# Kernel optimization log

Measured on AMD Instinct MI355X. Metric: run time of the kernel, lower is better.

## Reference

```python
import jax, jax.numpy as jnp
import numpy as np
from jax import lax

T = 2048          # tokens (batch*seq, module flattens to [-1, hidden])
H = 2048          # hidden_size
E = 32            # n_routed_experts
DF = 1024         # moe_intermediate_size
DS = 4096         # moe_shared_expert_intermediate_size
TOP_K = 6         # num_experts_per_tok
N_GROUP = 8
TOPK_GROUP = 4
SCALE = 2.5       # routed_scaling_factor
NORM_TOPK = True


def relu2(x):
    r = jax.nn.relu(x)
    return r * r


def setup_inputs() -> dict:
    key = jax.random.key(0)
    ks = jax.random.split(key, 7)
    s = 0.02
    return {
        "x": jax.random.normal(ks[0], (T, H), dtype=jnp.float32),
        "router_w": jax.random.normal(ks[1], (E, H), dtype=jnp.float32) * s,
        "router_b": jax.random.normal(ks[2], (E,), dtype=jnp.float32) * s,
        "w_up": jax.random.normal(ks[3], (E, H, DF), dtype=jnp.float32) * s,
        "w_down": jax.random.normal(ks[4], (E, DF, H), dtype=jnp.float32) * s,
        "shared_up": jax.random.normal(ks[5], (H, DS), dtype=jnp.float32) * s,
        "shared_down": jax.random.normal(ks[6], (DS, H), dtype=jnp.float32) * s,
    }


def _route(x, router_w, router_b):
    # router in fp32: logits -> sigmoid scores -> group-restricted top-k
    logits = x @ router_w.T                                  # [T, E]
    scores = jax.nn.sigmoid(logits)
    sfc = scores + router_b[None, :]                         # scores_for_choice
    gsize = E // N_GROUP
    grp = sfc.reshape(T, N_GROUP, gsize)
    group_scores = lax.top_k(grp, 2)[0].sum(-1)              # [T, n_group] sum of top-2
    _, gidx = lax.top_k(group_scores, TOPK_GROUP)            # [T, topk_group]
    group_mask = jax.nn.one_hot(gidx, N_GROUP, dtype=sfc.dtype).sum(1)  # [T, n_group]
    score_mask = jnp.repeat(group_mask, gsize, axis=1)       # [T, E]
    masked = jnp.where(score_mask > 0, sfc, 0.0)
    _, tidx = lax.top_k(masked, TOP_K)                       # [T, top_k]
    tw = jnp.take_along_axis(scores, tidx, axis=1)           # gather raw scores
    if NORM_TOPK:
        tw = tw / (tw.sum(-1, keepdims=True) + 1e-20)
    tw = tw * SCALE
    return tidx, tw


def reference(x, router_w, router_b, w_up, w_down, shared_up, shared_down):
    tidx, tw = _route(x, router_w, router_b)
    # dense combine weights [T, E]; equals sum of routed weights per expert
    combine = (jax.nn.one_hot(tidx, E, dtype=tw.dtype) * tw[..., None]).sum(1)
    # routed experts (no bias, so scaling before down_proj == scaling the output)
    h = jnp.einsum('td,edf->tef', x, w_up)                   # [T, E, DF]
    a = relu2(h) * combine[:, :, None]
    moe_out = jnp.einsum('tef,efd->td', a, w_down)           # [T, H]
    shared_out = relu2(x @ shared_up) @ shared_down
    return moe_out + shared_out
```

## Files before the change

kernel.cpp:

```cpp
#include <hip/hip_runtime.h>
#include <hip/hip_bf16.h>
#include <math.h>

#define T_TOK 2048
#define HID   2048
#define NE    32
#define DF    1024
#define DSZ   4096
#define TOPK  6
#define NGRP  8
#define TOPKG 4
#define RSCALE 2.5f
#define EXT_E 36
#define NSLOT 20480

typedef __attribute__((ext_vector_type(8))) short short8;
typedef __attribute__((ext_vector_type(4))) float f32x4;

typedef __attribute__((address_space(1))) const void gv1;
typedef __attribute__((address_space(3))) void lv3;

static __device__ __forceinline__ void gload16(const void* g, void* l) {
    __builtin_amdgcn_global_load_lds((gv1*)g, (lv3*)l, 16, 0, 0);
}

static __device__ __forceinline__ unsigned short f2b(float f) {
    union { float f; unsigned u; } v; v.f = f;
    unsigned r = v.u + 0x7fffu + ((v.u >> 16) & 1u);
    return (unsigned short)(r >> 16);
}

static __device__ __forceinline__ float b2f(unsigned short b) {
    union { float f; unsigned u; } v; v.u = ((unsigned)b) << 16;
    return v.f;
}

__global__ __launch_bounds__(256)
void router_kernel(const float* __restrict__ x, const float* __restrict__ rw,
                   const float* __restrict__ rb,
                   int* __restrict__ tidx, float* __restrict__ tw,
                   int* __restrict__ counts, unsigned short* __restrict__ xb) {
    __shared__ float xs[HID];
    __shared__ float part[256];
    __shared__ float scores[NE];
    __shared__ float sfc[NE];
    int t = blockIdx.x;
    int tid = threadIdx.x;
    for (int i = tid; i < HID / 4; i += 256) {
        ((float4*)xs)[i] = ((const float4*)(x + (size_t)t * HID))[i];
    }
    __syncthreads();
    {
        float4 a = ((const float4*)xs)[tid * 2];
        float4 b = ((const float4*)xs)[tid * 2 + 1];
        short8 o;
        o[0] = (short)f2b(a.x); o[1] = (short)f2b(a.y); o[2] = (short)f2b(a.z); o[3] = (short)f2b(a.w);
        o[4] = (short)f2b(b.x); o[5] = (short)f2b(b.y); o[6] = (short)f2b(b.z); o[7] = (short)f2b(b.w);
        *(short8*)(xb + (size_t)t * HID + tid * 8) = o;
    }
    int e = tid & 31, ch = tid >> 5;
    const float* w = rw + (size_t)e * HID + ch * 256;
    const float* xv = xs + ch * 256;
    float p = 0.f;
    #pragma unroll 8
    for (int k = 0; k < 256; ++k) p += xv[k] * w[k];
    part[tid] = p;
    __syncthreads();
    if (tid < 32) {
        float l = 0.f;
        #pragma unroll
        for (int c = 0; c < 8; ++c) l += part[c * 32 + tid];
        float s = 1.f / (1.f + expf(-l));
        scores[tid] = s;
        sfc[tid] = s + rb[tid];
    }
    __syncthreads();
    if (tid == 0) {
        float gs[NGRP];
        for (int g = 0; g < NGRP; ++g) {
            float v[4];
            for (int i = 0; i < 4; ++i) v[i] = sfc[g * 4 + i];
            int bi = 0;
            for (int i = 1; i < 4; ++i) if (v[i] > v[bi]) bi = i;
            float m1 = v[bi]; v[bi] = -INFINITY;
            int bj = 0;
            for (int i = 1; i < 4; ++i) if (v[i] > v[bj]) bj = i;
            gs[g] = m1 + v[bj];
        }
        bool gsel[NGRP];
        for (int g = 0; g < NGRP; ++g) gsel[g] = false;
        for (int k = 0; k < TOPKG; ++k) {
            int bi = -1; float b = -INFINITY;
            for (int g = 0; g < NGRP; ++g)
                if (!gsel[g] && gs[g] > b) { b = gs[g]; bi = g; }
            gsel[bi] = true;
        }
        float masked[NE];
        for (int i = 0; i < NE; ++i) masked[i] = gsel[i >> 2] ? sfc[i] : 0.0f;
        int sel[TOPK]; float wv[TOPK]; float wsum = 0.f;
        for (int k = 0; k < TOPK; ++k) {
            int bi = -1; float b = -INFINITY;
            for (int i = 0; i < NE; ++i)
                if (masked[i] > b) { b = masked[i]; bi = i; }
            masked[bi] = -INFINITY;
            sel[k] = bi; wv[k] = scores[bi]; wsum += wv[k];
        }
        float inv = RSCALE / (wsum + 1e-20f);
        for (int k = 0; k < TOPK; ++k) {
            tidx[t * TOPK + k] = sel[k];
            tw[t * TOPK + k] = wv[k] * inv;
            atomicAdd(&counts[sel[k]], 1);
        }
    }
}

__global__ void scan_kernel(const int* __restrict__ counts, int* __restrict__ offsets) {
    if (threadIdx.x == 0) {
        int a = 0;
        for (int e2 = 0; e2 < NE; ++e2) { offsets[e2] = a; a += counts[e2]; }
        offsets[NE] = a;
        for (int j = 1; j <= 4; ++j) offsets[NE + j] = 12288 + j * T_TOK;
    }
}

__global__ void scatter_kernel(const int* __restrict__ tidx, const float* __restrict__ tw,
                               const int* __restrict__ offsets, int* __restrict__ cursors,
                               int* __restrict__ perm, float* __restrict__ pw,
                               int* __restrict__ slot_of) {
    int t = blockIdx.x * blockDim.x + threadIdx.x;
    if (t >= T_TOK) return;
    for (int k = 0; k < TOPK; ++k) {
        int e = tidx[t * TOPK + k];
        int pos = atomicAdd(&cursors[e], 1);
        int slot = offsets[e] + pos;
        perm[slot] = t;
        pw[slot] = tw[t * TOPK + k];
        slot_of[t * TOPK + k] = slot;
    }
    #pragma unroll
    for (int j = 0; j < 4; ++j) {
        int slot = 12288 + j * T_TOK + t;
        perm[slot] = t;
        pw[slot] = 1.0f;
    }
}

static __device__ __forceinline__ void transpose_tile64(
        const float* __restrict__ src, unsigned short* __restrict__ dst,
        int rs, int Kd, int k0, int n0) {
    __shared__ float tl[64][65];
    int t = threadIdx.x;
    int r0 = t >> 4;
    int c4 = (t & 15) * 4;
    #pragma unroll
    for (int p = 0; p < 4; ++p) {
        int r = r0 + p * 16;
        float4 v = *(const float4*)(src + (size_t)(k0 + r) * rs + n0 + c4);
        tl[c4 + 0][r] = v.x;
        tl[c4 + 1][r] = v.y;
        tl[c4 + 2][r] = v.z;
        tl[c4 + 3][r] = v.w;
    }
    __syncthreads();
    int n = t >> 2;
    int kq = (t & 3) * 16;
    unsigned short o[16];
    #pragma unroll
    for (int i = 0; i < 16; ++i) o[i] = f2b(tl[n][kq + i]);
    unsigned short* d = dst + (size_t)(n0 + n) * Kd + k0 + kq;
    *(short8*)(d) = *(short8*)&o[0];
    *(short8*)(d + 8) = *(short8*)&o[8];
}

__global__ __launch_bounds__(256)
void transpose_all_kernel(const float* __restrict__ w_up, const float* __restrict__ sh_up,
                          const float* __restrict__ w_dn, const float* __restrict__ sh_dn,
                          unsigned short* __restrict__ bufU, unsigned short* __restrict__ bufD) {
    int z = blockIdx.y;
    int tile = blockIdx.x;
    if (z < EXT_E) {
        const float* src; int rs;
        if (z < NE) { src = w_up + (size_t)z * HID * DF; rs = DF; }
        else        { src = sh_up + (size_t)(z - NE) * DF; rs = DSZ; }
        int tn = tile & 15, tk = tile >> 4;
        transpose_tile64(src, bufU + (size_t)z * DF * HID, rs, HID, tk * 64, tn * 64);
    } else {
        int zz = z - EXT_E;
        const float* src = (zz < NE) ? (w_dn + (size_t)zz * DF * HID)
                                     : (sh_dn + (size_t)(zz - NE) * DF * HID);
        int tn = tile & 31, tk = tile >> 5;
        transpose_tile64(src, bufD + (size_t)zz * HID * DF, HID, DF, tk * 64, tn * 64);
    }
}

__global__ __launch_bounds__(256, 2)
void gemm_up_kernel(const unsigned short* __restrict__ xb, const unsigned short* __restrict__ bufU,
                    unsigned short* __restrict__ act, const int* __restrict__ offsets,
                    const int* __restrict__ perm, const float* __restrict__ pw) {
    constexpr int K = HID, N = DF;
    __shared__ __align__(16) char lds[32768];
    char* As = lds;
    char* Bs = lds + 16384;

    int tid = threadIdx.x;
    int lane = tid & 63, wvid = tid >> 6, wr = wvid >> 1, wc = wvid & 1;

    int bz = blockIdx.z;
    int off = offsets[bz], end = offsets[bz + 1];
    int row0 = off + blockIdx.y * 128;
    if (row0 >= end) return;
    int n0 = blockIdx.x * 128;

    int lr = lane >> 3;
    int csrc = (((lane & 7) ^ lr) << 4);
    size_t abyte[4], bbyte[4];
    int ldsoff[4];
    const char* Bb = (const char*)bufU + (size_t)bz * ((size_t)N * K * 2);
    #pragma unroll
    for (int p = 0; p < 4; ++p) {
        int r = p * 32 + wvid * 8 + lr;
        int gr = row0 + r;
        if (gr > end - 1) gr = end - 1;
        abyte[p] = (size_t)perm[gr] * (K * 2);
        bbyte[p] = (size_t)(n0 + r) * (K * 2);
        ldsoff[p] = (p * 32 + wvid * 8) * 128;
    }

    f32x4 acc[4][4] = {};
    for (int k0 = 0; k0 < K; k0 += 64) {
        __syncthreads();
        #pragma unroll
        for (int p = 0; p < 4; ++p) {
            gload16((const char*)xb + abyte[p] + k0 * 2 + csrc, As + ldsoff[p]);
            gload16(Bb + bbyte[p] + k0 * 2 + csrc, Bs + ldsoff[p]);
        }
        __syncthreads();
        #pragma unroll
        for (int ks = 0; ks < 2; ++ks) {
            int kg = lane >> 4, r16 = lane & 15;
            short8 af[4], bfr[4];
            #pragma unroll
            for (int m = 0; m < 4; ++m) {
                int r = wr * 64 + m * 16 + r16;
                af[m] = *(const short8*)(As + r * 128 + ((ks * 64 + kg * 16) ^ ((r & 7) << 4)));
            }
            #pragma unroll
            for (int n = 0; n < 4; ++n) {
                int c = wc * 64 + n * 16 + r16;
                bfr[n] = *(const short8*)(Bs + c * 128 + ((ks * 64 + kg * 16) ^ ((c & 7) << 4)));
            }
            #pragma unroll
            for (int m = 0; m < 4; ++m)
                #pragma unroll
                for (int n = 0; n < 4; ++n)
                    acc[m][n] = __builtin_amdgcn_mfma_f32_16x16x32_bf16(af[m], bfr[n], acc[m][n], 0, 0, 0);
        }
    }

    int r16 = lane & 15, rg = lane >> 4;
    #pragma unroll
    for (int m = 0; m < 4; ++m) {
        #pragma unroll
        for (int j = 0; j < 4; ++j) {
            int rr = row0 + wr * 64 + m * 16 + rg * 4 + j;
            if (rr < end) {
                float scale = pw[rr];
                #pragma unroll
                for (int n = 0; n < 4; ++n) {
                    int cc = n0 + wc * 64 + n * 16 + r16;
                    float v = acc[m][n][j];
                    v = v > 0.f ? v * v : 0.f;
                    act[(size_t)rr * N + cc] = f2b(v * scale);
                }
            }
        }
    }
}

__global__ __launch_bounds__(256, 2)
void gemm_down_kernel(const unsigned short* __restrict__ act, const unsigned short* __restrict__ bufD,
                      unsigned short* __restrict__ slotout, const int* __restrict__ offsets) {
    constexpr int K = DF, N = HID;
    __shared__ __align__(16) char lds[32768];
    char* As = lds;
    char* Bs = lds + 16384;

    int tid = threadIdx.x;
    int lane = tid & 63, wvid = tid >> 6, wr = wvid >> 1, wc = wvid & 1;

    int bz = blockIdx.z;
    int off = offsets[bz], end = offsets[bz + 1];
    int row0 = off + blockIdx.y * 128;
    if (row0 >= end) return;
    int n0 = blockIdx.x * 128;

    int lr = lane >> 3;
    int csrc = (((lane & 7) ^ lr) << 4);
    size_t abyte[4], bbyte[4];
    int ldsoff[4];
    const char* Bb = (const char*)bufD + (size_t)bz * ((size_t)N * K * 2);
    #pragma unroll
    for (int p = 0; p < 4; ++p) {
        int r = p * 32 + wvid * 8 + lr;
        int gr = row0 + r;
        if (gr > end - 1) gr = end - 1;
        abyte[p] = (size_t)gr * (K * 2);
        bbyte[p] = (size_t)(n0 + r) * (K * 2);
        ldsoff[p] = (p * 32 + wvid * 8) * 128;
    }

    f32x4 acc[4][4] = {};
    for (int k0 = 0; k0 < K; k0 += 64) {
        __syncthreads();
        #pragma unroll
        for (int p = 0; p < 4; ++p) {
            gload16((const char*)act + abyte[p] + k0 * 2 + csrc, As + ldsoff[p]);
            gload16(Bb + bbyte[p] + k0 * 2 + csrc, Bs + ldsoff[p]);
        }
        __syncthreads();
        #pragma unroll
        for (int ks = 0; ks < 2; ++ks) {
            int kg = lane >> 4, r16 = lane & 15;
            short8 af[4], bfr[4];
            #pragma unroll
            for (int m = 0; m < 4; ++m) {
                int r = wr * 64 + m * 16 + r16;
                af[m] = *(const short8*)(As + r * 128 + ((ks * 64 + kg * 16) ^ ((r & 7) << 4)));
            }
            #pragma unroll
            for (int n = 0; n < 4; ++n) {
                int c = wc * 64 + n * 16 + r16;
                bfr[n] = *(const short8*)(Bs + c * 128 + ((ks * 64 + kg * 16) ^ ((c & 7) << 4)));
            }
            #pragma unroll
            for (int m = 0; m < 4; ++m)
                #pragma unroll
                for (int n = 0; n < 4; ++n)
                    acc[m][n] = __builtin_amdgcn_mfma_f32_16x16x32_bf16(af[m], bfr[n], acc[m][n], 0, 0, 0);
        }
    }

    int r16 = lane & 15, rg = lane >> 4;
    #pragma unroll
    for (int m = 0; m < 4; ++m) {
        #pragma unroll
        for (int j = 0; j < 4; ++j) {
            int rr = row0 + wr * 64 + m * 16 + rg * 4 + j;
            if (rr < end) {
                #pragma unroll
                for (int n = 0; n < 4; ++n) {
                    int cc = n0 + wc * 64 + n * 16 + r16;
                    slotout[(size_t)rr * N + cc] = f2b(acc[m][n][j]);
                }
            }
        }
    }
}

__global__ void combine_kernel(const unsigned short* __restrict__ slotout,
                               const int* __restrict__ slot_of,
                               float* __restrict__ out) {
    int t = blockIdx.x, tid = threadIdx.x;
    int s[10];
    #pragma unroll
    for (int k = 0; k < TOPK; ++k) s[k] = slot_of[t * TOPK + k];
    #pragma unroll
    for (int j = 0; j < 4; ++j) s[TOPK + j] = 12288 + j * T_TOK + t;
    int c = tid * 8;
    float a[8] = {0.f, 0.f, 0.f, 0.f, 0.f, 0.f, 0.f, 0.f};
    #pragma unroll
    for (int k = 0; k < 10; ++k) {
        short8 v = *(const short8*)(slotout + (size_t)s[k] * HID + c);
        #pragma unroll
        for (int i = 0; i < 8; ++i) a[i] += b2f((unsigned short)v[i]);
    }
    *(float4*)(out + (size_t)t * HID + c) = make_float4(a[0], a[1], a[2], a[3]);
    *(float4*)(out + (size_t)t * HID + c + 4) = make_float4(a[4], a[5], a[6], a[7]);
}

extern "C" void kernel_launch(void* const* d_in, const int* in_sizes, int n_in,
                              void* d_out, int out_size, void* d_ws, size_t ws_size,
                              hipStream_t stream) {
    const float* x     = (const float*)d_in[0];
    const float* rw    = (const float*)d_in[1];
    const float* rb    = (const float*)d_in[2];
    const float* w_up  = (const float*)d_in[3];
    const float* w_dn  = (const float*)d_in[4];
    const float* sh_up = (const float*)d_in[5];
    const float* sh_dn = (const float*)d_in[6];
    float* out = (float*)d_out;
    char* ws = (char*)d_ws;

    int*   counts  = (int*)(ws);
    int*   cursors = (int*)(ws + 128);
    int*   offsets = (int*)(ws + 256);
    int*   tidx    = (int*)(ws + 1024);
    float* tw      = (float*)(ws + 50176);
    int*   slot_of = (int*)(ws + 99328);
    int*   perm    = (int*)(ws + 148480);
    float* pw      = (float*)(ws + 230400);
    unsigned short* xb   = (unsigned short*)(ws + 312320);
    unsigned short* act  = (unsigned short*)(ws + 8700928);
    unsigned short* bufU = (unsigned short*)(ws + 50643968);
    unsigned short* bufD = (unsigned short*)(ws + 201638912);
    unsigned short* slotout = (unsigned short*)(ws + 352633856);

    hipMemsetAsync(ws, 0, 256, stream);

    router_kernel<<<T_TOK, 256, 0, stream>>>(x, rw, rb, tidx, tw, counts, xb);
    scan_kernel<<<1, 64, 0, stream>>>(counts, offsets);
    scatter_kernel<<<(T_TOK + 255) / 256, 256, 0, stream>>>(tidx, tw, offsets, cursors,
                                                            perm, pw, slot_of);

    transpose_all_kernel<<<dim3(512, 2 * EXT_E), 256, 0, stream>>>(
        w_up, sh_up, w_dn, sh_dn, bufU, bufD);

    gemm_up_kernel<<<dim3(DF / 128, T_TOK / 128, EXT_E), 256, 0, stream>>>(
        xb, bufU, act, offsets, perm, pw);

    gemm_down_kernel<<<dim3(HID / 128, T_TOK / 128, EXT_E), 256, 0, stream>>>(
        act, bufD, slotout, offsets);

    combine_kernel<<<T_TOK, 256, 0, stream>>>(slotout, slot_of, out);
}
```

Before: 572.8 us.

## Fuse weight fp32-to-bf16 conversion into GEMMs using transposed LDS reads

Removes the separate transpose/convert pass over all expert and shared weights. Each GEMM now loads fp32 weight tiles directly, converts them to bf16 in registers, stores them row-major in LDS, and uses ds_read_b64_tr_b16 to produce the transposed MFMA B fragments. This avoids writing and rereading about 300MB of bf16 weight copies. In exchange, each GEMM block rereads fp32 weights, which doubles B-operand load bytes per tile and repeats the conversion across row tiles. B loads also become synchronous register loads instead of direct global-to-LDS loads.

Result: slower. 680.6 us (+18.8%).

```diff
diff --git a/kernel.cpp b/kernel.cpp
--- a/kernel.cpp
+++ b/kernel.cpp
@@ -15,6 +15,7 @@
 #define NSLOT 20480
 
 typedef __attribute__((ext_vector_type(8))) short short8;
+typedef __attribute__((ext_vector_type(4))) short short4v;
 typedef __attribute__((ext_vector_type(4))) float f32x4;
 
 typedef __attribute__((address_space(1))) const void gv1;
@@ -28,6 +29,12 @@
     union { float f; unsigned u; } v; v.f = f;
     unsigned r = v.u + 0x7fffu + ((v.u >> 16) & 1u);
     return (unsigned short)(r >> 16);
+}
+
+static __device__ __forceinline__ unsigned short b16(float f) {
+    union { __hip_bfloat16 h; unsigned short u; } c;
+    c.h = __float2bfloat16(f);
+    return c.u;
 }
 
 static __device__ __forceinline__ float b2f(unsigned short b) {
@@ -145,59 +152,14 @@
     }
 }
 
-static __device__ __forceinline__ void transpose_tile64(
-        const float* __restrict__ src, unsigned short* __restrict__ dst,
-        int rs, int Kd, int k0, int n0) {
-    __shared__ float tl[64][65];
-    int t = threadIdx.x;
-    int r0 = t >> 4;
-    int c4 = (t & 15) * 4;
-    #pragma unroll
-    for (int p = 0; p < 4; ++p) {
-        int r = r0 + p * 16;
-        float4 v = *(const float4*)(src + (size_t)(k0 + r) * rs + n0 + c4);
-        tl[c4 + 0][r] = v.x;
-        tl[c4 + 1][r] = v.y;
-        tl[c4 + 2][r] = v.z;
-        tl[c4 + 3][r] = v.w;
-    }
-    __syncthreads();
-    int n = t >> 2;
-    int kq = (t & 3) * 16;
-    unsigned short o[16];
-    #pragma unroll
-    for (int i = 0; i < 16; ++i) o[i] = f2b(tl[n][kq + i]);
-    unsigned short* d = dst + (size_t)(n0 + n) * Kd + k0 + kq;
-    *(short8*)(d) = *(short8*)&o[0];
-    *(short8*)(d + 8) = *(short8*)&o[8];
-}
-
-__global__ __launch_bounds__(256)
-void transpose_all_kernel(const float* __restrict__ w_up, const float* __restrict__ sh_up,
-                          const float* __restrict__ w_dn, const float* __restrict__ sh_dn,
-                          unsigned short* __restrict__ bufU, unsigned short* __restrict__ bufD) {
-    int z = blockIdx.y;
-    int tile = blockIdx.x;
-    if (z < EXT_E) {
-        const float* src; int rs;
-        if (z < NE) { src = w_up + (size_t)z * HID * DF; rs = DF; }
-        else        { src = sh_up + (size_t)(z - NE) * DF; rs = DSZ; }
-        int tn = tile & 15, tk = tile >> 4;
-        transpose_tile64(src, bufU + (size_t)z * DF * HID, rs, HID, tk * 64, tn * 64);
-    } else {
-        int zz = z - EXT_E;
-        const float* src = (zz < NE) ? (w_dn + (size_t)zz * DF * HID)
-                                     : (sh_dn + (size_t)(zz - NE) * DF * HID);
-        int tn = tile & 31, tk = tile >> 5;
-        transpose_tile64(src, bufD + (size_t)zz * HID * DF, HID, DF, tk * 64, tn * 64);
-    }
-}
-
+template<int MODE>
 __global__ __launch_bounds__(256, 2)
-void gemm_up_kernel(const unsigned short* __restrict__ xb, const unsigned short* __restrict__ bufU,
-                    unsigned short* __restrict__ act, const int* __restrict__ offsets,
+void gemm_tr_kernel(const unsigned short* __restrict__ Abuf,
+                    const float* __restrict__ Wmain, const float* __restrict__ Wsh,
+                    unsigned short* __restrict__ Cbuf, const int* __restrict__ offsets,
                     const int* __restrict__ perm, const float* __restrict__ pw) {
-    constexpr int K = HID, N = DF;
+    constexpr int K = (MODE == 0) ? HID : DF;
+    constexpr int N = (MODE == 0) ? DF : HID;
     __shared__ __align__(16) char lds[32768];
     char* As = lds;
     char* Bs = lds + 16384;
@@ -211,49 +173,80 @@
     if (row0 >= end) return;
     int n0 = blockIdx.x * 128;
 
+    const float* Bsrc; long ldb;
+    if (MODE == 0) {
+        if (bz < NE) { Bsrc = Wmain + (size_t)bz * HID * DF; ldb = DF; }
+        else         { Bsrc = Wsh + (size_t)(bz - NE) * DF;  ldb = DSZ; }
+    } else {
+        Bsrc = (bz < NE) ? (Wmain + (size_t)bz * DF * HID)
+                         : (Wsh + (size_t)(bz - NE) * DF * HID);
+        ldb = HID;
+    }
+
     int lr = lane >> 3;
     int csrc = (((lane & 7) ^ lr) << 4);
-    size_t abyte[4], bbyte[4];
+    size_t abyte[4];
     int ldsoff[4];
-    const char* Bb = (const char*)bufU + (size_t)bz * ((size_t)N * K * 2);
     #pragma unroll
     for (int p = 0; p < 4; ++p) {
         int r = p * 32 + wvid * 8 + lr;
         int gr = row0 + r;
         if (gr > end - 1) gr = end - 1;
-        abyte[p] = (size_t)perm[gr] * (K * 2);
-        bbyte[p] = (size_t)(n0 + r) * (K * 2);
+        int s = (MODE == 0) ? perm[gr] : gr;
+        abyte[p] = (size_t)s * (K * 2);
         ldsoff[p] = (p * 32 + wvid * 8) * 128;
     }
+
+    int kr0 = (tid & 3) + ((tid >> 6) & 1) * 4;
+    int nc  = ((tid >> 2) & 15) * 4 + (tid >> 7) * 64;
+    int bwbase = (kr0 >> 2) * 1024 + (nc >> 4) * 128 + (kr0 & 3) * 32 + (nc & 15) * 2;
+
+    unsigned bsb = (unsigned)(uintptr_t)(lv3*)Bs + (unsigned)((lane >> 4) * 2048 + (lane & 15) * 8);
 
     f32x4 acc[4][4] = {};
     for (int k0 = 0; k0 < K; k0 += 64) {
         __syncthreads();
         #pragma unroll
-        for (int p = 0; p < 4; ++p) {
-            gload16((const char*)xb + abyte[p] + k0 * 2 + csrc, As + ldsoff[p]);
-            gload16(Bb + bbyte[p] + k0 * 2 + csrc, Bs + ldsoff[p]);
+        for (int p = 0; p < 4; ++p)
+            gload16((const char*)Abuf + abyte[p] + k0 * 2 + csrc, As + ldsoff[p]);
+        {
+            const float* bp = Bsrc + (size_t)(k0 + kr0) * ldb + n0 + nc;
+            #pragma unroll
+            for (int p = 0; p < 8; ++p) {
+                float4 v = *(const float4*)(bp + (size_t)p * 8 * ldb);
+                unsigned short h[4] = { b16(v.x), b16(v.y), b16(v.z), b16(v.w) };
+                *(short4v*)(Bs + bwbase + p * 2048) = *(short4v*)h;
+            }
         }
         __syncthreads();
         #pragma unroll
         for (int ks = 0; ks < 2; ++ks) {
-            int kg = lane >> 4, r16 = lane & 15;
-            short8 af[4], bfr[4];
+            int r16 = lane & 15, kg = lane >> 4;
+            short8 af[4];
             #pragma unroll
             for (int m = 0; m < 4; ++m) {
                 int r = wr * 64 + m * 16 + r16;
                 af[m] = *(const short8*)(As + r * 128 + ((ks * 64 + kg * 16) ^ ((r & 7) << 4)));
             }
+            short4v t0[4], t1[4];
             #pragma unroll
             for (int n = 0; n < 4; ++n) {
-                int c = wc * 64 + n * 16 + r16;
-                bfr[n] = *(const short8*)(Bs + c * 128 + ((ks * 64 + kg * 16) ^ ((c & 7) << 4)));
-            }
+                unsigned a = bsb + ks * 8192 + (wc * 4 + n) * 128;
+                asm volatile("ds_read_b64_tr_b16 %0, %2\n\t"
+                             "ds_read_b64_tr_b16 %1, %2 offset:1024"
+                             : "=v"(t0[n]), "=v"(t1[n]) : "v"(a));
+            }
+            asm volatile("s_waitcnt lgkmcnt(0)" ::: "memory");
+            __builtin_amdgcn_sched_barrier(0);
             #pragma unroll
-            for (int m = 0; m < 4; ++m)
+            for (int n = 0; n < 4; ++n) {
+                short8 bfr;
+                bfr[0] = t0[n][0]; bfr[1] = t0[n][1]; bfr[2] = t0[n][2]; bfr[3] = t0[n][3];
+                bfr[4] = t1[n][0]; bfr[5] = t1[n][1]; bfr[6] = t1[n][2]; bfr[7] = t1[n][3];
                 #pragma unroll
-                for (int n = 0; n < 4; ++n)
-                    acc[m][n] = __builtin_amdgcn_mfma_f32_16x16x32_bf16(af[m], bfr[n], acc[m][n], 0, 0, 0);
+                for (int m = 0; m < 4; ++m)
+                    acc[m][n] = __builtin_amdgcn_mfma_f32_16x16x32_bf16(af[m], bfr, acc[m][n], 0, 0, 0);
+            }
         }
     }
 
@@ -264,93 +257,21 @@
         for (int j = 0; j < 4; ++j) {
             int rr = row0 + wr * 64 + m * 16 + rg * 4 + j;
             if (rr < end) {
-                float scale = pw[rr];
-                #pragma unroll
-                for (int n = 0; n < 4; ++n) {
-                    int cc = n0 + wc * 64 + n * 16 + r16;
-                    float v = acc[m][n][j];
-                    v = v > 0.f ? v * v : 0.f;
-                    act[(size_t)rr * N + cc] = f2b(v * scale);
-                }
-            }
-        }
-    }
-}
-
-__global__ __launch_bounds__(256, 2)
-void gemm_down_kernel(const unsigned short* __restrict__ act, const unsigned short* __restrict__ bufD,
-                      unsigned short* __restrict__ slotout, const int* __restrict__ offsets) {
-    constexpr int K = DF, N = HID;
-    __shared__ __align__(16) char lds[32768];
-    char* As = lds;
-    char* Bs = lds + 16384;
-
-    int tid = threadIdx.x;
-    int lane = tid & 63, wvid = tid >> 6, wr = wvid >> 1, wc = wvid & 1;
-
-    int bz = blockIdx.z;
-    int off = offsets[bz], end = offsets[bz + 1];
-    int row0 = off + blockIdx.y * 128;
-    if (row0 >= end) return;
-    int n0 = blockIdx.x * 128;
-
-    int lr = lane >> 3;
-    int csrc = (((lane & 7) ^ lr) << 4);
-    size_t abyte[4], bbyte[4];
-    int ldsoff[4];
-    const char* Bb = (const char*)bufD + (size_t)bz * ((size_t)N * K * 2);
-    #pragma unroll
-    for (int p = 0; p < 4; ++p) {
-        int r = p * 32 + wvid * 8 + lr;
-        int gr = row0 + r;
-        if (gr > end - 1) gr = end - 1;
-        abyte[p] = (size_t)gr * (K * 2);
-        bbyte[p] = (size_t)(n0 + r) * (K * 2);
-        ldsoff[p] = (p * 32 + wvid * 8) * 128;
-    }
-
-    f32x4 acc[4][4] = {};
-    for (int k0 = 0; k0 < K; k0 += 64) {
-        __syncthreads();
-        #pragma unroll
-        for (int p = 0; p < 4; ++p) {
-            gload16((const char*)act + abyte[p] + k0 * 2 + csrc, As + ldsoff[p]);
-            gload16(Bb + bbyte[p] + k0 * 2 + csrc, Bs + ldsoff[p]);
-        }
-        __syncthreads();
-        #pragma unroll
-        for (int ks = 0; ks < 2; ++ks) {
-            int kg = lane >> 4, r16 = lane & 15;
-            short8 af[4], bfr[4];
-            #pragma unroll
-            for (int m = 0; m < 4; ++m) {
-                int r = wr * 64 + m * 16 + r16;
-                af[m] = *(const short8*)(As + r * 128 + ((ks * 64 + kg * 16) ^ ((r & 7) << 4)));
-            }
-            #pragma unroll
-            for (int n = 0; n < 4; ++n) {
-                int c = wc * 64 + n * 16 + r16;
-                bfr[n] = *(const short8*)(Bs + c * 128 + ((ks * 64 + kg * 16) ^ ((c & 7) << 4)));
-            }
-            #pragma unroll
-            for (int m = 0; m < 4; ++m)
-                #pragma unroll
-                for (int n = 0; n < 4; ++n)
-                    acc[m][n] = __builtin_amdgcn_mfma_f32_16x16x32_bf16(af[m], bfr[n], acc[m][n], 0, 0, 0);
-        }
-    }
-
-    int r16 = lane & 15, rg = lane >> 4;
-    #pragma unroll
-    for (int m = 0; m < 4; ++m) {
-        #pragma unroll
-        for (int j = 0; j < 4; ++j) {
-            int rr = row0 + wr * 64 + m * 16 + rg * 4 + j;
-            if (rr < end) {
-                #pragma unroll
-                for (int n = 0; n < 4; ++n) {
-                    int cc = n0 + wc * 64 + n * 16 + r16;
-                    slotout[(size_t)rr * N + cc] = f2b(acc[m][n][j]);
+                if (MODE == 0) {
+                    float scale = pw[rr];
+                    #pragma unroll
+                    for (int n = 0; n < 4; ++n) {
+                        int cc = n0 + wc * 64 + n * 16 + r16;
+                        float v = acc[m][n][j];
+                        v = v > 0.f ? v * v : 0.f;
+                        Cbuf[(size_t)rr * N + cc] = f2b(v * scale);
+                    }
+                } else {
+                    #pragma unroll
+                    for (int n = 0; n < 4; ++n) {
+                        int cc = n0 + wc * 64 + n * 16 + r16;
+                        Cbuf[(size_t)rr * N + cc] = f2b(acc[m][n][j]);
+                    }
                 }
             }
         }
@@ -401,9 +322,7 @@
     float* pw      = (float*)(ws + 230400);
     unsigned short* xb   = (unsigned short*)(ws + 312320);
     unsigned short* act  = (unsigned short*)(ws + 8700928);
-    unsigned short* bufU = (unsigned short*)(ws + 50643968);
-    unsigned short* bufD = (unsigned short*)(ws + 201638912);
-    unsigned short* slotout = (unsigned short*)(ws + 352633856);
+    unsigned short* slotout = (unsigned short*)(ws + 50643968);
 
     hipMemsetAsync(ws, 0, 256, stream);
 
@@ -412,14 +331,11 @@
     scatter_kernel<<<(T_TOK + 255) / 256, 256, 0, stream>>>(tidx, tw, offsets, cursors,
                                                             perm, pw, slot_of);
 
-    transpose_all_kernel<<<dim3(512, 2 * EXT_E), 256, 0, stream>>>(
-        w_up, sh_up, w_dn, sh_dn, bufU, bufD);
-
-    gemm_up_kernel<<<dim3(DF / 128, T_TOK / 128, EXT_E), 256, 0, stream>>>(
-        xb, bufU, act, offsets, perm, pw);
-
-    gemm_down_kernel<<<dim3(HID / 128, T_TOK / 128, EXT_E), 256, 0, stream>>>(
-        act, bufD, slotout, offsets);
+    gemm_tr_kernel<0><<<dim3(DF / 128, T_TOK / 128, EXT_E), 256, 0, stream>>>(
+        xb, w_up, sh_up, act, offsets, perm, pw);
+
+    gemm_tr_kernel<1><<<dim3(HID / 128, T_TOK / 128, EXT_E), 256, 0, stream>>>(
+        act, w_dn, sh_dn, slotout, offsets, perm, pw);
 
     combine_kernel<<<T_TOK, 256, 0, stream>>>(slotout, slot_of, out);
 }
```

## Double-buffer LDS tiles in up and down expert GEMMs to overlap loads

Applied to the files above, without the earlier changes.

Both grouped GEMM kernels now use two 32KB LDS buffers. The next K-tile is prefetched with global_load_lds while MFMAs run on the current tile, which hides global memory latency and leaves one barrier per iteration instead of two. The cost is twice the LDS per block (64KB), which may limit occupancy below the two blocks requested in launch bounds. Correctness relies on the trailing barrier waiting for the async LDS loads to finish.

New measurement: 614.7 us. 7.3% more time.

```diff
diff --git a/kernel.cpp b/kernel.cpp
--- a/kernel.cpp
+++ b/kernel.cpp
@@ -198,9 +198,7 @@
                     unsigned short* __restrict__ act, const int* __restrict__ offsets,
                     const int* __restrict__ perm, const float* __restrict__ pw) {
     constexpr int K = HID, N = DF;
-    __shared__ __align__(16) char lds[32768];
-    char* As = lds;
-    char* Bs = lds + 16384;
+    __shared__ __align__(16) char lds[65536];
 
     int tid = threadIdx.x;
     int lane = tid & 63, wvid = tid >> 6, wr = wvid >> 1, wc = wvid & 1;
@@ -227,14 +225,27 @@
     }
 
     f32x4 acc[4][4] = {};
-    for (int k0 = 0; k0 < K; k0 += 64) {
-        __syncthreads();
-        #pragma unroll
-        for (int p = 0; p < 4; ++p) {
-            gload16((const char*)xb + abyte[p] + k0 * 2 + csrc, As + ldsoff[p]);
-            gload16(Bb + bbyte[p] + k0 * 2 + csrc, Bs + ldsoff[p]);
-        }
-        __syncthreads();
+    constexpr int NT = K / 64;
+    int cur = 0;
+    #pragma unroll
+    for (int p = 0; p < 4; ++p) {
+        gload16((const char*)xb + abyte[p] + csrc, lds + ldsoff[p]);
+        gload16(Bb + bbyte[p] + csrc, lds + 16384 + ldsoff[p]);
+    }
+    __syncthreads();
+
+    for (int t = 0; t < NT; ++t) {
+        char* As = lds + cur * 32768;
+        char* Bs = As + 16384;
+        if (t + 1 < NT) {
+            int k2 = (t + 1) * 128;
+            char* Ad = lds + (cur ^ 1) * 32768;
+            #pragma unroll
+            for (int p = 0; p < 4; ++p) {
+                gload16((const char*)xb + abyte[p] + k2 + csrc, Ad + ldsoff[p]);
+                gload16(Bb + bbyte[p] + k2 + csrc, Ad + 16384 + ldsoff[p]);
+            }
+        }
         #pragma unroll
         for (int ks = 0; ks < 2; ++ks) {
             int kg = lane >> 4, r16 = lane & 15;
@@ -255,6 +266,8 @@
                 for (int n = 0; n < 4; ++n)
                     acc[m][n] = __builtin_amdgcn_mfma_f32_16x16x32_bf16(af[m], bfr[n], acc[m][n], 0, 0, 0);
         }
+        __syncthreads();
+        cur ^= 1;
     }
 
     int r16 = lane & 15, rg = lane >> 4;
@@ -281,9 +294,7 @@
 void gemm_down_kernel(const unsigned short* __restrict__ act, const unsigned short* __restrict__ bufD,
                       unsigned short* __restrict__ slotout, const int* __restrict__ offsets) {
     constexpr int K = DF, N = HID;
-    __shared__ __align__(16) char lds[32768];
-    char* As = lds;
-    char* Bs = lds + 16384;
+    __shared__ __align__(16) char lds[65536];
 
     int tid = threadIdx.x;
     int lane = tid & 63, wvid = tid >> 6, wr = wvid >> 1, wc = wvid & 1;
@@ -310,14 +321,27 @@
     }
 
     f32x4 acc[4][4] = {};
-    for (int k0 = 0; k0 < K; k0 += 64) {
-        __syncthreads();
-        #pragma unroll
-        for (int p = 0; p < 4; ++p) {
-            gload16((const char*)act + abyte[p] + k0 * 2 + csrc, As + ldsoff[p]);
-            gload16(Bb + bbyte[p] + k0 * 2 + csrc, Bs + ldsoff[p]);
-        }
-        __syncthreads();
+    constexpr int NT = K / 64;
+    int cur = 0;
+    #pragma unroll
+    for (int p = 0; p < 4; ++p) {
+        gload16((const char*)act + abyte[p] + csrc, lds + ldsoff[p]);
+        gload16(Bb + bbyte[p] + csrc, lds + 16384 + ldsoff[p]);
+    }
+    __syncthreads();
+
+    for (int t = 0; t < NT; ++t) {
+        char* As = lds + cur * 32768;
+        char* Bs = As + 16384;
+        if (t + 1 < NT) {
+            int k2 = (t + 1) * 128;
+            char* Ad = lds + (cur ^ 1) * 32768;
+            #pragma unroll
+            for (int p = 0; p < 4; ++p) {
+                gload16((const char*)act + abyte[p] + k2 + csrc, Ad + ldsoff[p]);
+                gload16(Bb + bbyte[p] + k2 + csrc, Ad + 16384 + ldsoff[p]);
+            }
+        }
         #pragma unroll
         for (int ks = 0; ks < 2; ++ks) {
             int kg = lane >> 4, r16 = lane & 15;
@@ -338,6 +362,8 @@
                 for (int n = 0; n < 4; ++n)
                     acc[m][n] = __builtin_amdgcn_mfma_f32_16x16x32_bf16(af[m], bfr[n], acc[m][n], 0, 0, 0);
         }
+        __syncthreads();
+        cur ^= 1;
     }
 
     int r16 = lane & 15, rg = lane >> 4;
```

## Overlap down-weight transpose with up-projection GEMM in one interleaved launch

Applied to the files above, without the earlier changes.

Splits the weight transpose so that only the up-projection weights are transposed before the up GEMM. The down-projection transpose tiles are interleaved with up-GEMM tiles in a single fused launch, four transpose blocks per GEMM block. The goal is to overlap the memory-bound fp32-to-bf16 transpose with the compute-bound GEMM and remove one launch plus its serialization. The cost is a shared LDS allocation sized for the GEMM, which may lower transpose occupancy, and mixed block types that could unbalance scheduling.

Measured after the change: 564.3 us, median of 2. About the same (-1.5%).

```diff
diff --git a/kernel.cpp b/kernel.cpp
--- a/kernel.cpp
+++ b/kernel.cpp
@@ -147,8 +147,8 @@
 
 static __device__ __forceinline__ void transpose_tile64(
         const float* __restrict__ src, unsigned short* __restrict__ dst,
-        int rs, int Kd, int k0, int n0) {
-    __shared__ float tl[64][65];
+        int rs, int Kd, int k0, int n0, char* smem) {
+    float (*tl)[65] = (float(*)[65])smem;
     int t = threadIdx.x;
     int r0 = t >> 4;
     int c4 = (t & 15) * 4;
@@ -173,43 +173,36 @@
 }
 
 __global__ __launch_bounds__(256)
-void transpose_all_kernel(const float* __restrict__ w_up, const float* __restrict__ sh_up,
-                          const float* __restrict__ w_dn, const float* __restrict__ sh_dn,
-                          unsigned short* __restrict__ bufU, unsigned short* __restrict__ bufD) {
+void transpose_up_kernel(const float* __restrict__ w_up, const float* __restrict__ sh_up,
+                         unsigned short* __restrict__ bufU) {
+    __shared__ __align__(16) char smem[16640];
     int z = blockIdx.y;
+    const float* src; int rs;
+    if (z < NE) { src = w_up + (size_t)z * HID * DF; rs = DF; }
+    else        { src = sh_up + (size_t)(z - NE) * DF; rs = DSZ; }
     int tile = blockIdx.x;
-    if (z < EXT_E) {
-        const float* src; int rs;
-        if (z < NE) { src = w_up + (size_t)z * HID * DF; rs = DF; }
-        else        { src = sh_up + (size_t)(z - NE) * DF; rs = DSZ; }
-        int tn = tile & 15, tk = tile >> 4;
-        transpose_tile64(src, bufU + (size_t)z * DF * HID, rs, HID, tk * 64, tn * 64);
-    } else {
-        int zz = z - EXT_E;
-        const float* src = (zz < NE) ? (w_dn + (size_t)zz * DF * HID)
-                                     : (sh_dn + (size_t)(zz - NE) * DF * HID);
-        int tn = tile & 31, tk = tile >> 5;
-        transpose_tile64(src, bufD + (size_t)zz * HID * DF, HID, DF, tk * 64, tn * 64);
-    }
-}
-
-__global__ __launch_bounds__(256, 2)
-void gemm_up_kernel(const unsigned short* __restrict__ xb, const unsigned short* __restrict__ bufU,
-                    unsigned short* __restrict__ act, const int* __restrict__ offsets,
-                    const int* __restrict__ perm, const float* __restrict__ pw) {
+    int tn = tile & 15, tk = tile >> 4;
+    transpose_tile64(src, bufU + (size_t)z * DF * HID, rs, HID, tk * 64, tn * 64, smem);
+}
+
+static __device__ void gemm_up_body(int bx, int by, int bz,
+                                    const unsigned short* __restrict__ xb,
+                                    const unsigned short* __restrict__ bufU,
+                                    unsigned short* __restrict__ act,
+                                    const int* __restrict__ offsets,
+                                    const int* __restrict__ perm,
+                                    const float* __restrict__ pw, char* lds) {
     constexpr int K = HID, N = DF;
-    __shared__ __align__(16) char lds[32768];
     char* As = lds;
     char* Bs = lds + 16384;
 
     int tid = threadIdx.x;
     int lane = tid & 63, wvid = tid >> 6, wr = wvid >> 1, wc = wvid & 1;
 
-    int bz = blockIdx.z;
     int off = offsets[bz], end = offsets[bz + 1];
-    int row0 = off + blockIdx.y * 128;
+    int row0 = off + by * 128;
     if (row0 >= end) return;
-    int n0 = blockIdx.x * 128;
+    int n0 = bx * 128;
 
     int lr = lane >> 3;
     int csrc = (((lane & 7) ^ lr) << 4);
@@ -275,6 +268,30 @@
             }
         }
     }
+}
+
+__global__ __launch_bounds__(256, 2)
+void gemm_up_tdn_kernel(const unsigned short* __restrict__ xb,
+                        const unsigned short* __restrict__ bufU,
+                        unsigned short* __restrict__ act,
+                        const int* __restrict__ offsets, const int* __restrict__ perm,
+                        const float* __restrict__ pw,
+                        const float* __restrict__ w_dn, const float* __restrict__ sh_dn,
+                        unsigned short* __restrict__ bufD) {
+    __shared__ __align__(16) char smem[32768];
+    int bid = blockIdx.x;
+    if (bid % 5 != 0) {
+        int tile = bid - bid / 5 - 1;
+        int tz = tile >> 9;
+        int rem = tile & 511;
+        int tn = rem & 31, tk = rem >> 5;
+        const float* src = (tz < NE) ? (w_dn + (size_t)tz * DF * HID)
+                                     : (sh_dn + (size_t)(tz - NE) * DF * HID);
+        transpose_tile64(src, bufD + (size_t)tz * HID * DF, HID, DF, tk * 64, tn * 64, smem);
+        return;
+    }
+    int g = bid / 5;
+    gemm_up_body(g & 7, (g >> 3) & 15, g >> 7, xb, bufU, act, offsets, perm, pw, smem);
 }
 
 __global__ __launch_bounds__(256, 2)
@@ -412,11 +429,10 @@
     scatter_kernel<<<(T_TOK + 255) / 256, 256, 0, stream>>>(tidx, tw, offsets, cursors,
                                                             perm, pw, slot_of);
 
-    transpose_all_kernel<<<dim3(512, 2 * EXT_E), 256, 0, stream>>>(
-        w_up, sh_up, w_dn, sh_dn, bufU, bufD);
-
-    gemm_up_kernel<<<dim3(DF / 128, T_TOK / 128, EXT_E), 256, 0, stream>>>(
-        xb, bufU, act, offsets, perm, pw);
+    transpose_up_kernel<<<dim3(512, EXT_E), 256, 0, stream>>>(w_up, sh_up, bufU);
+
+    gemm_up_tdn_kernel<<<23040, 256, 0, stream>>>(xb, bufU, act, offsets, perm, pw,
+                                                  w_dn, sh_dn, bufD);
 
     gemm_down_kernel<<<dim3(HID / 128, T_TOK / 128, EXT_E), 256, 0, stream>>>(
         act, bufD, slotout, offsets);
```
